# Optimization experiments

Measured on AMD Instinct MI355X. Metric: run time of the kernel, lower is better.

Reference implementation:

```python
import jax, jax.numpy as jnp
import numpy as np

GRID_SIZE = 5
SPLINE_ORDER = 3
N_COEFF = GRID_SIZE + SPLINE_ORDER  # 8 basis functions per input feature
D_MODEL = 1024
D_FF = 4096


def make_grid(in_features):
    # uniform grid on [-1, 1] extended by spline_order knots each side
    h = 2.0 / GRID_SIZE
    g = np.arange(-SPLINE_ORDER, GRID_SIZE + SPLINE_ORDER + 1, dtype=np.float32) * h - 1.0
    return jnp.asarray(np.tile(g[None, :], (in_features, 1)))  # (in, G + 2k + 1)


def b_splines(x, grid):
    # x: (N, in) -> (N, in, G + k) via Cox-de Boor recursion
    xe = x[..., None]
    bases = ((xe >= grid[:, :-1]) & (xe < grid[:, 1:])).astype(x.dtype)
    for j in range(1, SPLINE_ORDER + 1):
        left = (xe - grid[:, : -(j + 1)]) / (grid[:, j:-1] - grid[:, : -(j + 1)])
        right = (grid[:, j + 1 :] - xe) / (grid[:, j + 1 :] - grid[:, 1:-j])
        bases = left * bases[..., :-1] + right * bases[..., 1:]
    return bases


def kan_linear(x, base_w, spline_w, grid):
    # x: (N, in); base_w: (out, in); spline_w: (out, in, C)
    base = jax.nn.silu(x) @ base_w.T
    b = b_splines(x, grid)                      # (N, in, C)
    spl = jnp.einsum('nic,oic->no', b, spline_w)
    return base + spl


def setup_inputs() -> dict:
    key = jax.random.key(0)
    ks = jax.random.split(key, 7)
    s_in = 1.0 / np.sqrt(D_MODEL)
    s_ff = 1.0 / np.sqrt(D_FF)
    return {
        'x': jax.random.normal(ks[0], (2, 2048, D_MODEL), jnp.float32),
        'base_w1': jax.random.normal(ks[1], (D_FF, D_MODEL), jnp.float32) * s_in,
        'spline_w1': jax.random.normal(ks[2], (D_FF, D_MODEL, N_COEFF), jnp.float32) * s_in * 0.1,
        'base_w2': jax.random.normal(ks[3], (D_FF, D_MODEL), jnp.float32) * s_in,
        'spline_w2': jax.random.normal(ks[4], (D_FF, D_MODEL, N_COEFF), jnp.float32) * s_in * 0.1,
        'base_w3': jax.random.normal(ks[5], (D_MODEL, D_FF), jnp.float32) * s_ff,
        'spline_w3': jax.random.normal(ks[6], (D_MODEL, D_FF, N_COEFF), jnp.float32) * s_ff * 0.1,
        'grid_in': make_grid(D_MODEL),
        'grid_ff': make_grid(D_FF),
    }


def reference(x, base_w1, spline_w1, base_w2, spline_w2, base_w3, spline_w3, grid_in, grid_ff):
    shp = x.shape
    x2 = x.reshape(-1, shp[-1])                      # (N, d_model)
    h = kan_linear(x2, base_w1, spline_w1, grid_in) * kan_linear(x2, base_w2, spline_w2, grid_in)
    out = kan_linear(h, base_w3, spline_w3, grid_ff)
    return out.reshape(shp)
```

## Files before the change

### kernel.cpp

```cpp
#include <hip/hip_runtime.h>
#include <hip/hip_bf16.h>
#include <cstdint>
#include <cstddef>
#include <type_traits>


#define D_MODEL 1024
#define D_FF    4096
#define NTOK    4096
#define NC      9
#define K1      (D_MODEL * NC)
#define K3      (D_FF * NC)
#define SPLITK2 16
#define CHUNK   1024

typedef __attribute__((ext_vector_type(8))) short bf16x8;
typedef __attribute__((ext_vector_type(4))) float f32x4;

__device__ __forceinline__ unsigned short bf16b(float f) {
  __hip_bfloat16 h = __float2bfloat16(f);
  return __builtin_bit_cast(unsigned short, h);
}

__device__ __forceinline__ void kan_feat_u(float x, unsigned short* dst) {
  float s = x / (1.0f + __expf(-x));
  float B[11];
#pragma unroll
  for (int j = 0; j < 11; ++j) {
    float gj = -2.2f + 0.4f * j;
    B[j] = (x >= gj && x < gj + 0.4f) ? 1.0f : 0.0f;
  }
#pragma unroll
  for (int p = 1; p <= 3; ++p) {
    float inv = 1.0f / (0.4f * p);
#pragma unroll
    for (int i = 0; i + p < 11; ++i) {
      float gi = -2.2f + 0.4f * i;
      B[i] = (x - gi) * inv * B[i] + ((gi + 0.4f + 0.4f * p) - x) * inv * B[i + 1];
    }
  }
  dst[0] = bf16b(s);
#pragma unroll
  for (int c = 0; c < 8; ++c) dst[1 + c] = bf16b(B[c]);
}

__global__ void pack_kan_w(const float* __restrict__ bw, const float* __restrict__ sw,
                           __hip_bfloat16* __restrict__ W, int K, int inShift,
                           size_t oBase, size_t totalPairs) {
  size_t t = (size_t)blockIdx.x * blockDim.x + threadIdx.x;
  if (t >= totalPairs) return;
  size_t o = t >> (inShift - 1);
  size_t ip = (t & (((size_t)1 << (inShift - 1)) - 1)) * 2;
  size_t e0 = (o << inShift) + ip;
  float2 b = *(const float2*)(bw + e0);
  const float4* sp = (const float4*)(sw + e0 * 8);
  float4 s0 = sp[0], s1 = sp[1], s2 = sp[2], s3 = sp[3];
  unsigned short h[18];
  h[0] = bf16b(b.x);
  h[1] = bf16b(s0.x); h[2] = bf16b(s0.y); h[3] = bf16b(s0.z); h[4] = bf16b(s0.w);
  h[5] = bf16b(s1.x); h[6] = bf16b(s1.y); h[7] = bf16b(s1.z); h[8] = bf16b(s1.w);
  h[9] = bf16b(b.y);
  h[10] = bf16b(s2.x); h[11] = bf16b(s2.y); h[12] = bf16b(s2.z); h[13] = bf16b(s2.w);
  h[14] = bf16b(s3.x); h[15] = bf16b(s3.y); h[16] = bf16b(s3.z); h[17] = bf16b(s3.w);
  uint32_t* dst = (uint32_t*)(W + (oBase + o) * (size_t)K + ip * NC);
#pragma unroll
  for (int k = 0; k < 9; ++k) dst[k] = (uint32_t)h[2 * k] | ((uint32_t)h[2 * k + 1] << 16);
}

__global__ void build_a1(const float* __restrict__ x, __hip_bfloat16* __restrict__ A1) {
  size_t t = (size_t)blockIdx.x * blockDim.x + threadIdx.x;
  if (t >= (size_t)NTOK * D_MODEL / 2) return;
  size_t n = t >> 9;
  size_t ip = (t & 511) * 2;
  float2 xv = *(const float2*)(x + n * D_MODEL + ip);
  unsigned short h[18];
  kan_feat_u(xv.x, h);
  kan_feat_u(xv.y, h + 9);
  uint32_t* dst = (uint32_t*)(A1 + n * (size_t)K1 + ip * NC);
#pragma unroll
  for (int k = 0; k < 9; ++k) dst[k] = (uint32_t)h[2 * k] | ((uint32_t)h[2 * k + 1] << 16);
}

template <typename HT>
__global__ void glu_a3(const HT* __restrict__ Hc, __hip_bfloat16* __restrict__ A3c) {
  size_t t = (size_t)blockIdx.x * blockDim.x + threadIdx.x;
  if (t >= (size_t)CHUNK * D_FF / 2) return;
  size_t n = t >> 11;
  size_t jp = (t & 2047) * 2;
  float a0, a1, c0, c1;
  if constexpr (std::is_same<HT, float>::value) {
    float2 u = *(const float2*)(Hc + n * 8192 + jp);
    float2 v = *(const float2*)(Hc + n * 8192 + 4096 + jp);
    a0 = u.x; a1 = u.y; c0 = v.x; c1 = v.y;
  } else {
    a0 = __bfloat162float(Hc[n * 8192 + jp]);
    a1 = __bfloat162float(Hc[n * 8192 + jp + 1]);
    c0 = __bfloat162float(Hc[n * 8192 + 4096 + jp]);
    c1 = __bfloat162float(Hc[n * 8192 + 4096 + jp + 1]);
  }
  unsigned short h[18];
  kan_feat_u(a0 * c0, h);
  kan_feat_u(a1 * c1, h + 9);
  uint32_t* dst = (uint32_t*)(A3c + n * (size_t)K3 + jp * NC);
#pragma unroll
  for (int k = 0; k < 9; ++k) dst[k] = (uint32_t)h[2 * k] | ((uint32_t)h[2 * k + 1] << 16);
}

#define STAGE_A(Ts)                                                                      \
  {                                                                                      \
    const int _sl = ((Ts) & 3) * 32768;                                                  \
    const size_t _ko = (size_t)(Ts) * 64;                                                \
    __builtin_amdgcn_global_load_lds(                                                    \
        (const __attribute__((address_space(1))) void*)(gA0 + _ko),                      \
        (__attribute__((address_space(3))) void*)(lds_raw + _sl + dA0), 16, 0, 0);       \
    __builtin_amdgcn_global_load_lds(                                                    \
        (const __attribute__((address_space(1))) void*)(gA1 + _ko),                      \
        (__attribute__((address_space(3))) void*)(lds_raw + _sl + dA1), 16, 0, 0);       \
  }
#define STAGE_B(Ts)                                                                      \
  {                                                                                      \
    const int _sl = ((Ts) & 3) * 32768;                                                  \
    const size_t _ko = (size_t)(Ts) * 64;                                                \
    __builtin_amdgcn_global_load_lds(                                                    \
        (const __attribute__((address_space(1))) void*)(gB0 + _ko),                      \
        (__attribute__((address_space(3))) void*)(lds_raw + _sl + dB0), 16, 0, 0);       \
    __builtin_amdgcn_global_load_lds(                                                    \
        (const __attribute__((address_space(1))) void*)(gB1 + _ko),                      \
        (__attribute__((address_space(3))) void*)(lds_raw + _sl + dB1), 16, 0, 0);       \
  }

template <typename CT>
__global__ __launch_bounds__(512, 2) void gemm256(
    const __hip_bfloat16* __restrict__ A, const __hip_bfloat16* __restrict__ Bw,
    CT* __restrict__ Cp, int N, int K, int kLen) {
  __shared__ __align__(16) char lds_raw[4 * 32768];

  const int tid = threadIdx.x;
  const int wid = tid >> 6, lane = tid & 63;
  const int wr = wid >> 2, wc = wid & 3;

  const int nwg = gridDim.x * gridDim.y;
  const int orig = blockIdx.y * gridDim.x + blockIdx.x;
  const int q = nwg >> 3, r = nwg & 7;
  const int xcd = orig & 7, lid = orig >> 3;
  const int wg = (xcd < r ? xcd * (q + 1) : r * (q + 1) + (xcd - r) * q) + lid;
  const int bx = wg % gridDim.x, by = wg / gridDim.x;

  const size_t brow = (size_t)by * 256;
  const size_t bcol = (size_t)bx * 256;
  const int kStart = (int)blockIdx.z * kLen;
  const int NT = kLen / 32;

  const int kbx = (lane & 3) ^ ((lane >> 3) & 3);
  const int rsub = lane >> 2;
  const char* gA0 = (const char*)A +
      ((brow + (size_t)(wid * 16 + rsub)) * (size_t)K + kStart + kbx * 8) * 2;
  const char* gA1 = (const char*)A +
      ((brow + 128 + (size_t)(wid * 16 + rsub)) * (size_t)K + kStart + kbx * 8) * 2;
  const char* gB0 = (const char*)Bw +
      ((bcol + (size_t)(wid * 16 + rsub)) * (size_t)K + kStart + kbx * 8) * 2;
  const char* gB1 = (const char*)Bw +
      ((bcol + 128 + (size_t)(wid * 16 + rsub)) * (size_t)K + kStart + kbx * 8) * 2;
  const int dA0 = wid * 1024;
  const int dA1 = 8192 + wid * 1024;
  const int dB0 = 16384 + wid * 1024;
  const int dB1 = 24576 + wid * 1024;

  const int fkb = (lane >> 4) ^ ((lane >> 1) & 3);
  const int aoff = (wr * 128 + (lane & 15)) * 64 + fkb * 16;
  const int boff = 16384 + (wc * 64 + (lane & 15)) * 64 + fkb * 16;

  f32x4 acc[8][4] = {};

  STAGE_A(0); STAGE_B(0);
  STAGE_A(1); STAGE_B(1);
  STAGE_A(2); STAGE_B(2);
  asm volatile("s_waitcnt vmcnt(8)" ::: "memory");
  __builtin_amdgcn_s_barrier();

  for (int T = 0; T < NT; ++T) {
    const int sl = (T & 3) * 32768;

    bf16x8 af0[4], bfr[4];
#pragma unroll
    for (int mf = 0; mf < 4; ++mf)
      af0[mf] = *(const bf16x8*)(lds_raw + sl + aoff + mf * 1024);
#pragma unroll
    for (int nf = 0; nf < 4; ++nf)
      bfr[nf] = *(const bf16x8*)(lds_raw + sl + boff + nf * 1024);
    if (T + 3 < NT) STAGE_A(T + 3);
    __builtin_amdgcn_s_barrier();
    asm volatile("s_waitcnt lgkmcnt(0)" ::: "memory");
    __builtin_amdgcn_sched_barrier(0);
    __builtin_amdgcn_s_setprio(1);
#pragma unroll
    for (int mf = 0; mf < 4; ++mf)
#pragma unroll
      for (int nf = 0; nf < 4; ++nf)
        acc[mf][nf] =
            __builtin_amdgcn_mfma_f32_16x16x32_bf16(af0[mf], bfr[nf], acc[mf][nf], 0, 0, 0);
    __builtin_amdgcn_s_setprio(0);
    __builtin_amdgcn_s_barrier();

    bf16x8 af1[4];
#pragma unroll
    for (int mf = 0; mf < 4; ++mf)
      af1[mf] = *(const bf16x8*)(lds_raw + sl + aoff + (mf + 4) * 1024);
    if (T + 3 < NT) STAGE_B(T + 3);
    __builtin_amdgcn_s_barrier();
    asm volatile("s_waitcnt lgkmcnt(0)" ::: "memory");
    __builtin_amdgcn_sched_barrier(0);
    __builtin_amdgcn_s_setprio(1);
#pragma unroll
    for (int mf = 0; mf < 4; ++mf)
#pragma unroll
      for (int nf = 0; nf < 4; ++nf)
        acc[mf + 4][nf] =
            __builtin_amdgcn_mfma_f32_16x16x32_bf16(af1[mf], bfr[nf], acc[mf + 4][nf], 0, 0, 0);
    __builtin_amdgcn_s_setprio(0);

    if (T + 4 <= NT) {
      asm volatile("s_waitcnt vmcnt(8)" ::: "memory");
    } else if (T + 3 == NT) {
      asm volatile("s_waitcnt vmcnt(4)" ::: "memory");
    } else if (T + 2 == NT) {
      asm volatile("s_waitcnt vmcnt(0)" ::: "memory");
    }
    __builtin_amdgcn_s_barrier();
  }

#pragma unroll
  for (int mf = 0; mf < 8; ++mf)
#pragma unroll
    for (int nf = 0; nf < 4; ++nf) {
      const size_t r0 = brow + wr * 128 + mf * 16 + (lane >> 4) * 4;
      const size_t c0 = bcol + wc * 64 + nf * 16 + (lane & 15);
      const size_t M = (size_t)gridDim.y * 256;
      CT* C = Cp + (size_t)blockIdx.z * M * (size_t)N;
#pragma unroll
      for (int rr = 0; rr < 4; ++rr) {
        float v = acc[mf][nf][rr];
        if constexpr (std::is_same<CT, float>::value)
          C[(r0 + rr) * (size_t)N + c0] = v;
        else
          C[(r0 + rr) * (size_t)N + c0] = __float2bfloat16(v);
      }
    }
}

__global__ void reduceK(const float* __restrict__ P, float* __restrict__ out, size_t quarter) {
  size_t t = (size_t)blockIdx.x * blockDim.x + threadIdx.x;
  if (t >= quarter) return;
  const float4* p = (const float4*)P;
  float4 a = p[t];
#pragma unroll
  for (int s = 1; s < SPLITK2; ++s) {
    float4 b = p[(size_t)s * quarter + t];
    a.x += b.x; a.y += b.y; a.z += b.z; a.w += b.w;
  }
  ((float4*)out)[t] = a;
}

extern "C" void kernel_launch(void* const* d_in, const int* in_sizes, int n_in,
                              void* d_out, int out_size, void* d_ws, size_t ws_size,
                              hipStream_t stream) {
  const float* x   = (const float*)d_in[0];
  const float* bw1 = (const float*)d_in[1];
  const float* sw1 = (const float*)d_in[2];
  const float* bw2 = (const float*)d_in[3];
  const float* sw2 = (const float*)d_in[4];
  const float* bw3 = (const float*)d_in[5];
  const float* sw3 = (const float*)d_in[6];
  float* out = (float*)d_out;
  char* ws = (char*)d_ws;

  const size_t W12_B  = (size_t)8192 * K1 * 2;
  const size_t A1_B   = (size_t)NTOK * K1 * 2;
  const size_t A3C_B  = (size_t)CHUNK * K3 * 2;
  const size_t HF32_B = (size_t)NTOK * 8192 * 4;

  const bool hF32 = ws_size >= W12_B + A1_B + HF32_B;

  __hip_bfloat16* W12 = (__hip_bfloat16*)(ws);
  __hip_bfloat16* A1  = (__hip_bfloat16*)(ws + W12_B);
  __hip_bfloat16* W3  = A1;
  void*           Hv  = (void*)(ws + W12_B + A1_B);
  __hip_bfloat16* A3c = (__hip_bfloat16*)(ws);
  float*          Par = (float*)(ws + A3C_B);

  {
    size_t pairs = (size_t)D_FF * D_MODEL / 2;
    int blocks = (int)((pairs + 255) / 256);
    pack_kan_w<<<blocks, 256, 0, stream>>>(bw1, sw1, W12, K1, 10, 0, pairs);
    pack_kan_w<<<blocks, 256, 0, stream>>>(bw2, sw2, W12, K1, 10, 4096, pairs);
  }
  {
    size_t pairs = (size_t)NTOK * D_MODEL / 2;
    build_a1<<<(int)((pairs + 255) / 256), 256, 0, stream>>>(x, A1);
  }
  if (hF32)
    gemm256<float><<<dim3(8192 / 256, NTOK / 256, 1), 512, 0, stream>>>(
        A1, W12, (float*)Hv, 8192, K1, K1);
  else
    gemm256<__hip_bfloat16><<<dim3(8192 / 256, NTOK / 256, 1), 512, 0, stream>>>(
        A1, W12, (__hip_bfloat16*)Hv, 8192, K1, K1);
  {
    size_t pairs = (size_t)D_MODEL * D_FF / 2;
    pack_kan_w<<<(int)((pairs + 255) / 256), 256, 0, stream>>>(bw3, sw3, W3, K3, 12, 0, pairs);
  }
  for (int c = 0; c < NTOK / CHUNK; ++c) {
    {
      size_t pairs = (size_t)CHUNK * D_FF / 2;
      int blocks = (int)((pairs + 255) / 256);
      if (hF32)
        glu_a3<float><<<blocks, 256, 0, stream>>>(
            (const float*)Hv + (size_t)c * CHUNK * 8192, A3c);
      else
        glu_a3<__hip_bfloat16><<<blocks, 256, 0, stream>>>(
            (const __hip_bfloat16*)Hv + (size_t)c * CHUNK * 8192, A3c);
    }
    gemm256<float><<<dim3(D_MODEL / 256, CHUNK / 256, SPLITK2), 512, 0, stream>>>(
        A3c, W3, Par, D_MODEL, K3, K3 / SPLITK2);
    {
      size_t quarter = (size_t)CHUNK * D_MODEL / 4;
      reduceK<<<(int)((quarter + 255) / 256), 256, 0, stream>>>(
          Par, out + (size_t)c * CHUNK * D_MODEL, quarter);
    }
  }
}
```

Baseline: 1.184 ms.

## Double-buffer register fragments and prefetch next tile's LDS reads during MFMA

Restructures the GEMM main loop so the LDS fragment reads for tile T+1 are issued into a second register set while the MFMAs for tile T run, using ping-pong register buffers and a loop unrolled by two. The A and B global-to-LDS staging is merged into one macro issued once per tile, and each tile now needs two barriers instead of four. The goal is to hide LDS read latency behind matrix math and cut synchronisation. In exchange it holds twice as many fragment registers, which may push register use past what the 2-blocks-per-SM launch bound allows. The unroll by two also assumes NT is even.

```diff
diff --git a/kernel.cpp b/kernel.cpp
--- a/kernel.cpp
+++ b/kernel.cpp
@@ -106,7 +106,7 @@
   for (int k = 0; k < 9; ++k) dst[k] = (uint32_t)h[2 * k] | ((uint32_t)h[2 * k + 1] << 16);
 }
 
-#define STAGE_A(Ts)                                                                      \
+#define STAGE(Ts)                                                                        \
   {                                                                                      \
     const int _sl = ((Ts) & 3) * 32768;                                                  \
     const size_t _ko = (size_t)(Ts) * 64;                                                \
@@ -116,17 +116,43 @@
     __builtin_amdgcn_global_load_lds(                                                    \
         (const __attribute__((address_space(1))) void*)(gA1 + _ko),                      \
         (__attribute__((address_space(3))) void*)(lds_raw + _sl + dA1), 16, 0, 0);       \
-  }
-#define STAGE_B(Ts)                                                                      \
-  {                                                                                      \
-    const int _sl = ((Ts) & 3) * 32768;                                                  \
-    const size_t _ko = (size_t)(Ts) * 64;                                                \
     __builtin_amdgcn_global_load_lds(                                                    \
         (const __attribute__((address_space(1))) void*)(gB0 + _ko),                      \
         (__attribute__((address_space(3))) void*)(lds_raw + _sl + dB0), 16, 0, 0);       \
     __builtin_amdgcn_global_load_lds(                                                    \
         (const __attribute__((address_space(1))) void*)(gB1 + _ko),                      \
         (__attribute__((address_space(3))) void*)(lds_raw + _sl + dB1), 16, 0, 0);       \
+  }
+
+#define READ_FRAGS(Ts, AF, BF)                                                           \
+  {                                                                                      \
+    const int _sr = ((Ts) & 3) * 32768;                                                  \
+    _Pragma("unroll") for (int _mf = 0; _mf < 8; ++_mf)                                  \
+        AF[_mf] = *(const bf16x8*)(lds_raw + _sr + aoff + _mf * 1024);                   \
+    _Pragma("unroll") for (int _nf = 0; _nf < 4; ++_nf)                                  \
+        BF[_nf] = *(const bf16x8*)(lds_raw + _sr + boff + _nf * 1024);                   \
+  }
+
+#define TILE_BODY(T, AC, BC, AN, BN)                                                     \
+  {                                                                                      \
+    if ((T) + 3 < NT) STAGE((T) + 3);                                                    \
+    if ((T) + 3 < NT) {                                                                  \
+      asm volatile("s_waitcnt vmcnt(8)" ::: "memory");                                   \
+    } else if ((T) + 3 == NT) {                                                          \
+      asm volatile("s_waitcnt vmcnt(4)" ::: "memory");                                   \
+    } else if ((T) + 2 == NT) {                                                          \
+      asm volatile("s_waitcnt vmcnt(0)" ::: "memory");                                   \
+    }                                                                                    \
+    __builtin_amdgcn_s_barrier();                          \
+    if ((T) + 1 < NT) READ_FRAGS((T) + 1, AN, BN);                                       \
+    __builtin_amdgcn_s_setprio(1);                                                       \
+    _Pragma("unroll") for (int _m = 0; _m < 8; ++_m)                                     \
+        _Pragma("unroll") for (int _n = 0; _n < 4; ++_n)                                 \
+            acc[_m][_n] = __builtin_amdgcn_mfma_f32_16x16x32_bf16(                       \
+                AC[_m], BC[_n], acc[_m][_n], 0, 0, 0);                                   \
+    __builtin_amdgcn_s_setprio(0);                                                       \
+    asm volatile("s_waitcnt lgkmcnt(0)" ::: "memory");         \
+    __builtin_amdgcn_s_barrier();                                                        \
   }
 
 template <typename CT>
@@ -171,62 +197,18 @@
   const int boff = 16384 + (wc * 64 + (lane & 15)) * 64 + fkb * 16;
 
   f32x4 acc[8][4] = {};
-
-  STAGE_A(0); STAGE_B(0);
-  STAGE_A(1); STAGE_B(1);
-  STAGE_A(2); STAGE_B(2);
+  bf16x8 aP[8], bP[4], aQ[8], bQ[4];
+
+  STAGE(0);
+  STAGE(1);
+  STAGE(2);
   asm volatile("s_waitcnt vmcnt(8)" ::: "memory");
   __builtin_amdgcn_s_barrier();
-
-  for (int T = 0; T < NT; ++T) {
-    const int sl = (T & 3) * 32768;
-
-    bf16x8 af0[4], bfr[4];
-#pragma unroll
-    for (int mf = 0; mf < 4; ++mf)
-      af0[mf] = *(const bf16x8*)(lds_raw + sl + aoff + mf * 1024);
-#pragma unroll
-    for (int nf = 0; nf < 4; ++nf)
-      bfr[nf] = *(const bf16x8*)(lds_raw + sl + boff + nf * 1024);
-    if (T + 3 < NT) STAGE_A(T + 3);
-    __builtin_amdgcn_s_barrier();
-    asm volatile("s_waitcnt lgkmcnt(0)" ::: "memory");
-    __builtin_amdgcn_sched_barrier(0);
-    __builtin_amdgcn_s_setprio(1);
-#pragma unroll
-    for (int mf = 0; mf < 4; ++mf)
-#pragma unroll
-      for (int nf = 0; nf < 4; ++nf)
-        acc[mf][nf] =
-            __builtin_amdgcn_mfma_f32_16x16x32_bf16(af0[mf], bfr[nf], acc[mf][nf], 0, 0, 0);
-    __builtin_amdgcn_s_setprio(0);
-    __builtin_amdgcn_s_barrier();
-
-    bf16x8 af1[4];
-#pragma unroll
-    for (int mf = 0; mf < 4; ++mf)
-      af1[mf] = *(const bf16x8*)(lds_raw + sl + aoff + (mf + 4) * 1024);
-    if (T + 3 < NT) STAGE_B(T + 3);
-    __builtin_amdgcn_s_barrier();
-    asm volatile("s_waitcnt lgkmcnt(0)" ::: "memory");
-    __builtin_amdgcn_sched_barrier(0);
-    __builtin_amdgcn_s_setprio(1);
-#pragma unroll
-    for (int mf = 0; mf < 4; ++mf)
-#pragma unroll
-      for (int nf = 0; nf < 4; ++nf)
-        acc[mf + 4][nf] =
-            __builtin_amdgcn_mfma_f32_16x16x32_bf16(af1[mf], bfr[nf], acc[mf + 4][nf], 0, 0, 0);
-    __builtin_amdgcn_s_setprio(0);
-
-    if (T + 4 <= NT) {
-      asm volatile("s_waitcnt vmcnt(8)" ::: "memory");
-    } else if (T + 3 == NT) {
-      asm volatile("s_waitcnt vmcnt(4)" ::: "memory");
-    } else if (T + 2 == NT) {
-      asm volatile("s_waitcnt vmcnt(0)" ::: "memory");
-    }
-    __builtin_amdgcn_s_barrier();
+  READ_FRAGS(0, aP, bP);
+
+  for (int T = 0; T < NT; T += 2) {
+    TILE_BODY(T, aP, bP, aQ, bQ);
+    TILE_BODY(T + 1, aQ, bQ, aP, bP);
   }
 
 #pragma unroll
```

Result: slower. 1.221 ms (+3.1%).

## Fuse GLU product and KAN feature build into first GEMM epilogue

Applied to the files above, without the earlier changes.

Interleaves the W1 and W2 rows so each GEMM tile holds matching pairs of outputs, computes their product in the epilogue via a lane shuffle, and writes the layer-3 KAN features straight from the tile through LDS. This removes the fp32 hidden-buffer round trip, the separate glu_a3 kernels and the chunk loop. The second GEMM then runs over all tokens with split-K 4 instead of 16, which shrinks the partial-sum reduction. The main loop is also reworked to issue all A/B staging loads at once with a single barrier per K-step, dropping the half-step barriers, at the cost of more live fragment registers and less overlap between loads and MFMA.

```diff
diff --git a/kernel.cpp b/kernel.cpp
--- a/kernel.cpp
+++ b/kernel.cpp
@@ -12,6 +12,7 @@
 #define K1      (D_MODEL * NC)
 #define K3      (D_FF * NC)
 #define SPLITK2 16
+#define SPLITKF 4
 #define CHUNK   1024
 
 typedef __attribute__((ext_vector_type(8))) short bf16x8;
@@ -46,7 +47,7 @@
 
 __global__ void pack_kan_w(const float* __restrict__ bw, const float* __restrict__ sw,
                            __hip_bfloat16* __restrict__ W, int K, int inShift,
-                           size_t oBase, size_t totalPairs) {
+                           int rowMul, int rowBase, size_t totalPairs) {
   size_t t = (size_t)blockIdx.x * blockDim.x + threadIdx.x;
   if (t >= totalPairs) return;
   size_t o = t >> (inShift - 1);
@@ -62,7 +63,7 @@
   h[9] = bf16b(b.y);
   h[10] = bf16b(s2.x); h[11] = bf16b(s2.y); h[12] = bf16b(s2.z); h[13] = bf16b(s2.w);
   h[14] = bf16b(s3.x); h[15] = bf16b(s3.y); h[16] = bf16b(s3.z); h[17] = bf16b(s3.w);
-  uint32_t* dst = (uint32_t*)(W + (oBase + o) * (size_t)K + ip * NC);
+  uint32_t* dst = (uint32_t*)(W + (o * rowMul + rowBase) * (size_t)K + ip * NC);
 #pragma unroll
   for (int k = 0; k < 9; ++k) dst[k] = (uint32_t)h[2 * k] | ((uint32_t)h[2 * k + 1] << 16);
 }
@@ -106,7 +107,7 @@
   for (int k = 0; k < 9; ++k) dst[k] = (uint32_t)h[2 * k] | ((uint32_t)h[2 * k + 1] << 16);
 }
 
-#define STAGE_A(Ts)                                                                      \
+#define STAGE(Ts)                                                                        \
   {                                                                                      \
     const int _sl = ((Ts) & 3) * 32768;                                                  \
     const size_t _ko = (size_t)(Ts) * 64;                                                \
@@ -116,11 +117,6 @@
     __builtin_amdgcn_global_load_lds(                                                    \
         (const __attribute__((address_space(1))) void*)(gA1 + _ko),                      \
         (__attribute__((address_space(3))) void*)(lds_raw + _sl + dA1), 16, 0, 0);       \
-  }
-#define STAGE_B(Ts)                                                                      \
-  {                                                                                      \
-    const int _sl = ((Ts) & 3) * 32768;                                                  \
-    const size_t _ko = (size_t)(Ts) * 64;                                                \
     __builtin_amdgcn_global_load_lds(                                                    \
         (const __attribute__((address_space(1))) void*)(gB0 + _ko),                      \
         (__attribute__((address_space(3))) void*)(lds_raw + _sl + dB0), 16, 0, 0);       \
@@ -129,10 +125,11 @@
         (__attribute__((address_space(3))) void*)(lds_raw + _sl + dB1), 16, 0, 0);       \
   }
 
-template <typename CT>
+template <typename CT, bool FUSE>
 __global__ __launch_bounds__(512, 2) void gemm256(
     const __hip_bfloat16* __restrict__ A, const __hip_bfloat16* __restrict__ Bw,
-    CT* __restrict__ Cp, int N, int K, int kLen) {
+    CT* __restrict__ Cp, int N, int K, int kLen,
+    __hip_bfloat16* __restrict__ A3out) {
   __shared__ __align__(16) char lds_raw[4 * 32768];
 
   const int tid = threadIdx.x;
@@ -172,51 +169,31 @@
 
   f32x4 acc[8][4] = {};
 
-  STAGE_A(0); STAGE_B(0);
-  STAGE_A(1); STAGE_B(1);
-  STAGE_A(2); STAGE_B(2);
+  STAGE(0);
+  STAGE(1);
+  STAGE(2);
   asm volatile("s_waitcnt vmcnt(8)" ::: "memory");
   __builtin_amdgcn_s_barrier();
 
   for (int T = 0; T < NT; ++T) {
+    if (T + 3 < NT) STAGE(T + 3);
+
     const int sl = (T & 3) * 32768;
-
-    bf16x8 af0[4], bfr[4];
-#pragma unroll
-    for (int mf = 0; mf < 4; ++mf)
-      af0[mf] = *(const bf16x8*)(lds_raw + sl + aoff + mf * 1024);
+    bf16x8 af[8], bfr[4];
+#pragma unroll
+    for (int mf = 0; mf < 8; ++mf)
+      af[mf] = *(const bf16x8*)(lds_raw + sl + aoff + mf * 1024);
 #pragma unroll
     for (int nf = 0; nf < 4; ++nf)
       bfr[nf] = *(const bf16x8*)(lds_raw + sl + boff + nf * 1024);
-    if (T + 3 < NT) STAGE_A(T + 3);
-    __builtin_amdgcn_s_barrier();
-    asm volatile("s_waitcnt lgkmcnt(0)" ::: "memory");
-    __builtin_amdgcn_sched_barrier(0);
+
     __builtin_amdgcn_s_setprio(1);
 #pragma unroll
-    for (int mf = 0; mf < 4; ++mf)
+    for (int mf = 0; mf < 8; ++mf)
 #pragma unroll
       for (int nf = 0; nf < 4; ++nf)
         acc[mf][nf] =
-            __builtin_amdgcn_mfma_f32_16x16x32_bf16(af0[mf], bfr[nf], acc[mf][nf], 0, 0, 0);
-    __builtin_amdgcn_s_setprio(0);
-    __builtin_amdgcn_s_barrier();
-
-    bf16x8 af1[4];
-#pragma unroll
-    for (int mf = 0; mf < 4; ++mf)
-      af1[mf] = *(const bf16x8*)(lds_raw + sl + aoff + (mf + 4) * 1024);
-    if (T + 3 < NT) STAGE_B(T + 3);
-    __builtin_amdgcn_s_barrier();
-    asm volatile("s_waitcnt lgkmcnt(0)" ::: "memory");
-    __builtin_amdgcn_sched_barrier(0);
-    __builtin_amdgcn_s_setprio(1);
-#pragma unroll
-    for (int mf = 0; mf < 4; ++mf)
-#pragma unroll
-      for (int nf = 0; nf < 4; ++nf)
-        acc[mf + 4][nf] =
-            __builtin_amdgcn_mfma_f32_16x16x32_bf16(af1[mf], bfr[nf], acc[mf + 4][nf], 0, 0, 0);
+            __builtin_amdgcn_mfma_f32_16x16x32_bf16(af[mf], bfr[nf], acc[mf][nf], 0, 0, 0);
     __builtin_amdgcn_s_setprio(0);
 
     if (T + 4 <= NT) {
@@ -226,35 +203,75 @@
     } else if (T + 2 == NT) {
       asm volatile("s_waitcnt vmcnt(0)" ::: "memory");
     }
+    asm volatile("s_waitcnt lgkmcnt(0)" ::: "memory");
     __builtin_amdgcn_s_barrier();
   }
 
-#pragma unroll
-  for (int mf = 0; mf < 8; ++mf)
-#pragma unroll
-    for (int nf = 0; nf < 4; ++nf) {
-      const size_t r0 = brow + wr * 128 + mf * 16 + (lane >> 4) * 4;
-      const size_t c0 = bcol + wc * 64 + nf * 16 + (lane & 15);
-      const size_t M = (size_t)gridDim.y * 256;
-      CT* C = Cp + (size_t)blockIdx.z * M * (size_t)N;
-#pragma unroll
-      for (int rr = 0; rr < 4; ++rr) {
-        float v = acc[mf][nf][rr];
-        if constexpr (std::is_same<CT, float>::value)
-          C[(r0 + rr) * (size_t)N + c0] = v;
-        else
-          C[(r0 + rr) * (size_t)N + c0] = __float2bfloat16(v);
+  if constexpr (FUSE) {
+    float* gbuf = (float*)lds_raw;
+#pragma unroll
+    for (int mf = 0; mf < 8; ++mf) {
+      const int s = wr * 8 + mf;
+#pragma unroll
+      for (int nf = 0; nf < 4; ++nf) {
+#pragma unroll
+        for (int rr = 0; rr < 4; ++rr) {
+          float v = acc[mf][nf][rr];
+          float w = __shfl_xor(v, 1, 64);
+          if (!(lane & 1)) {
+            const int r4 = (lane >> 4) * 4 + rr;
+            const int ploc = wc * 32 + nf * 8 + ((lane & 14) >> 1);
+            gbuf[s * 2048 + r4 * 128 + ploc] = v * w;
+          }
+        }
       }
     }
-}
-
-__global__ void reduceK(const float* __restrict__ P, float* __restrict__ out, size_t quarter) {
+    __builtin_amdgcn_s_barrier();
+    const int p2 = tid & 63;
+    const int rb = tid >> 6;
+    for (int k = 0; k < 32; ++k) {
+      const int rr_ = rb + 8 * k;
+      const int s = rr_ >> 4, rl = rr_ & 15;
+      float g0 = gbuf[s * 2048 + rl * 128 + 2 * p2];
+      float g1 = gbuf[s * 2048 + rl * 128 + 2 * p2 + 1];
+      unsigned short h[18];
+      kan_feat_u(g0, h);
+      kan_feat_u(g1, h + 9);
+      const size_t n = brow + rr_;
+      const size_t pg = (bcol >> 1) + 2 * p2;
+      uint32_t* dst = (uint32_t*)(A3out + n * (size_t)K3 + pg * NC);
+#pragma unroll
+      for (int qq = 0; qq < 9; ++qq)
+        dst[qq] = (uint32_t)h[2 * qq] | ((uint32_t)h[2 * qq + 1] << 16);
+    }
+  } else {
+#pragma unroll
+    for (int mf = 0; mf < 8; ++mf)
+#pragma unroll
+      for (int nf = 0; nf < 4; ++nf) {
+        const size_t r0 = brow + wr * 128 + mf * 16 + (lane >> 4) * 4;
+        const size_t c0 = bcol + wc * 64 + nf * 16 + (lane & 15);
+        const size_t M = (size_t)gridDim.y * 256;
+        CT* C = Cp + (size_t)blockIdx.z * M * (size_t)N;
+#pragma unroll
+        for (int rr = 0; rr < 4; ++rr) {
+          float v = acc[mf][nf][rr];
+          if constexpr (std::is_same<CT, float>::value)
+            C[(r0 + rr) * (size_t)N + c0] = v;
+          else
+            C[(r0 + rr) * (size_t)N + c0] = __float2bfloat16(v);
+        }
+      }
+  }
+}
+
+__global__ void reduceK(const float* __restrict__ P, float* __restrict__ out,
+                        size_t quarter, int nslice) {
   size_t t = (size_t)blockIdx.x * blockDim.x + threadIdx.x;
   if (t >= quarter) return;
   const float4* p = (const float4*)P;
   float4 a = p[t];
-#pragma unroll
-  for (int s = 1; s < SPLITK2; ++s) {
+  for (int s = 1; s < nslice; ++s) {
     float4 b = p[(size_t)s * quarter + t];
     a.x += b.x; a.y += b.y; a.z += b.z; a.w += b.w;
   }
@@ -276,55 +293,66 @@
 
   const size_t W12_B  = (size_t)8192 * K1 * 2;
   const size_t A1_B   = (size_t)NTOK * K1 * 2;
+  const size_t A3F_B  = (size_t)NTOK * K3 * 2;
   const size_t A3C_B  = (size_t)CHUNK * K3 * 2;
   const size_t HF32_B = (size_t)NTOK * 8192 * 4;
 
-  const bool hF32 = ws_size >= W12_B + A1_B + HF32_B;
+  const bool fused = ws_size >= W12_B + A1_B + A3F_B;
+  const bool hF32  = ws_size >= W12_B + A1_B + HF32_B;
 
   __hip_bfloat16* W12 = (__hip_bfloat16*)(ws);
   __hip_bfloat16* A1  = (__hip_bfloat16*)(ws + W12_B);
   __hip_bfloat16* W3  = A1;
-  void*           Hv  = (void*)(ws + W12_B + A1_B);
-  __hip_bfloat16* A3c = (__hip_bfloat16*)(ws);
-  float*          Par = (float*)(ws + A3C_B);
-
-  {
-    size_t pairs = (size_t)D_FF * D_MODEL / 2;
-    int blocks = (int)((pairs + 255) / 256);
-    pack_kan_w<<<blocks, 256, 0, stream>>>(bw1, sw1, W12, K1, 10, 0, pairs);
-    pack_kan_w<<<blocks, 256, 0, stream>>>(bw2, sw2, W12, K1, 10, 4096, pairs);
-  }
-  {
-    size_t pairs = (size_t)NTOK * D_MODEL / 2;
-    build_a1<<<(int)((pairs + 255) / 256), 256, 0, stream>>>(x, A1);
-  }
-  if (hF32)
-    gemm256<float><<<dim3(8192 / 256, NTOK / 256, 1), 512, 0, stream>>>(
-        A1, W12, (float*)Hv, 8192, K1, K1);
-  else
-    gemm256<__hip_bfloat16><<<dim3(8192 / 256, NTOK / 256, 1), 512, 0, stream>>>(
-        A1, W12, (__hip_bfloat16*)Hv, 8192, K1, K1);
-  {
-    size_t pairs = (size_t)D_MODEL * D_FF / 2;
-    pack_kan_w<<<(int)((pairs + 255) / 256), 256, 0, stream>>>(bw3, sw3, W3, K3, 12, 0, pairs);
-  }
-  for (int c = 0; c < NTOK / CHUNK; ++c) {
-    {
-      size_t pairs = (size_t)CHUNK * D_FF / 2;
-      int blocks = (int)((pairs + 255) / 256);
+
+  size_t pairs12 = (size_t)D_FF * D_MODEL / 2;
+  int blocks12 = (int)((pairs12 + 255) / 256);
+  size_t pairs3 = (size_t)D_MODEL * D_FF / 2;
+  int blocks3 = (int)((pairs3 + 255) / 256);
+  size_t pairsA1 = (size_t)NTOK * D_MODEL / 2;
+
+  if (fused) {
+    __hip_bfloat16* A3f = (__hip_bfloat16*)(ws + W12_B + A1_B);
+    float*          Par = (float*)(ws);
+
+    pack_kan_w<<<blocks12, 256, 0, stream>>>(bw1, sw1, W12, K1, 10, 2, 0, pairs12);
+    pack_kan_w<<<blocks12, 256, 0, stream>>>(bw2, sw2, W12, K1, 10, 2, 1, pairs12);
+    build_a1<<<(int)((pairsA1 + 255) / 256), 256, 0, stream>>>(x, A1);
+    gemm256<float, true><<<dim3(8192 / 256, NTOK / 256, 1), 512, 0, stream>>>(
+        A1, W12, nullptr, 8192, K1, K1, A3f);
+    pack_kan_w<<<blocks3, 256, 0, stream>>>(bw3, sw3, W3, K3, 12, 1, 0, pairs3);
+    gemm256<float, false><<<dim3(D_MODEL / 256, NTOK / 256, SPLITKF), 512, 0, stream>>>(
+        A3f, W3, Par, D_MODEL, K3, K3 / SPLITKF, nullptr);
+    size_t quarter = (size_t)NTOK * D_MODEL / 4;
+    reduceK<<<(int)((quarter + 255) / 256), 256, 0, stream>>>(Par, out, quarter, SPLITKF);
+  } else {
+    void*           Hv  = (void*)(ws + W12_B + A1_B);
+    __hip_bfloat16* A3c = (__hip_bfloat16*)(ws);
+    float*          Par = (float*)(ws + A3C_B);
+
+    pack_kan_w<<<blocks12, 256, 0, stream>>>(bw1, sw1, W12, K1, 10, 1, 0, pairs12);
+    pack_kan_w<<<blocks12, 256, 0, stream>>>(bw2, sw2, W12, K1, 10, 1, 4096, pairs12);
+    build_a1<<<(int)((pairsA1 + 255) / 256), 256, 0, stream>>>(x, A1);
+    if (hF32)
+      gemm256<float, false><<<dim3(8192 / 256, NTOK / 256, 1), 512, 0, stream>>>(
+          A1, W12, (float*)Hv, 8192, K1, K1, nullptr);
+    else
+      gemm256<__hip_bfloat16, false><<<dim3(8192 / 256, NTOK / 256, 1), 512, 0, stream>>>(
+          A1, W12, (__hip_bfloat16*)Hv, 8192, K1, K1, nullptr);
+    pack_kan_w<<<blocks3, 256, 0, stream>>>(bw3, sw3, W3, K3, 12, 1, 0, pairs3);
+    for (int c = 0; c < NTOK / CHUNK; ++c) {
+      size_t pairsG = (size_t)CHUNK * D_FF / 2;
+      int blocksG = (int)((pairsG + 255) / 256);
       if (hF32)
-        glu_a3<float><<<blocks, 256, 0, stream>>>(
+        glu_a3<float><<<blocksG, 256, 0, stream>>>(
             (const float*)Hv + (size_t)c * CHUNK * 8192, A3c);
       else
-        glu_a3<__hip_bfloat16><<<blocks, 256, 0, stream>>>(
+        glu_a3<__hip_bfloat16><<<blocksG, 256, 0, stream>>>(
             (const __hip_bfloat16*)Hv + (size_t)c * CHUNK * 8192, A3c);
-    }
-    gemm256<float><<<dim3(D_MODEL / 256, CHUNK / 256, SPLITK2), 512, 0, stream>>>(
-        A3c, W3, Par, D_MODEL, K3, K3 / SPLITK2);
-    {
+      gemm256<float, false><<<dim3(D_MODEL / 256, CHUNK / 256, SPLITK2), 512, 0, stream>>>(
+          A3c, W3, Par, D_MODEL, K3, K3 / SPLITK2, nullptr);
       size_t quarter = (size_t)CHUNK * D_MODEL / 4;
       reduceK<<<(int)((quarter + 255) / 256), 256, 0, stream>>>(
-          Par, out + (size_t)c * CHUNK * D_MODEL, quarter);
-    }
-  }
-}
+          Par, out + (size_t)c * CHUNK * D_MODEL, quarter, SPLITK2);
+    }
+  }
+}
```

New measurement: 1.078 ms. 9.0% less time.
